# Kernel tuning notes

Measured on AMD Instinct MI355X. Metric: run time of the kernel, lower is better.

The kernel has to match this reference:

```python
import jax, jax.numpy as jnp
import numpy as np

B, T, C = 4, 2048, 1024
E, K, HID = 8, 2, 4096  # n_expert, top-k, mult*dim


def setup_inputs() -> dict:
    key = jax.random.key(0)
    ks = jax.random.split(key, 9)
    s = 1.0 / np.sqrt(C)
    sh = 1.0 / np.sqrt(HID)
    return {
        "x": jax.random.normal(ks[0], (B, T, C), jnp.float32),
        "wg_w": jax.random.normal(ks[1], (C, E), jnp.float32) * s,
        "wg_b": jnp.zeros((E,), jnp.float32),
        "w1": jax.random.normal(ks[2], (E, C, HID), jnp.float32) * s,
        "b1": jnp.zeros((E, HID), jnp.float32),
        "w3": jax.random.normal(ks[3], (E, C, HID), jnp.float32) * s,
        "b3": jnp.zeros((E, HID), jnp.float32),
        "w2": jax.random.normal(ks[4], (E, HID, C), jnp.float32) * sh,
        "b2": jnp.zeros((E, C), jnp.float32),
    }


def reference(x, wg_w, wg_b, w1, b1, w3, b3, w2, b2):
    Bx, Tx, Cx = x.shape
    xf = x.reshape(-1, Cx)                       # (S, C)
    S = xf.shape[0]
    # --- TopKGate ---
    logits = xf @ wg_w + wg_b                    # (S, E)
    probs = jax.nn.softmax(logits, axis=-1)
    vals, idx = jax.lax.top_k(probs, K)          # (S, K)
    importance = probs.mean(axis=0)              # (E,)
    load = jnp.zeros((E,), probs.dtype).at[idx[:, 0]].add(1.0) / S
    aux = E * (importance * load).sum()
    # per-token per-expert combine weight (top-k ids are unique per row)
    w_full = jnp.zeros((S, E), probs.dtype).at[jnp.arange(S)[:, None], idx].add(vals)
    # --- experts: SwiGLU FFN, loop over small fixed E ---
    y = jnp.zeros_like(xf)
    for e in range(E):
        h = jax.nn.silu(xf @ w1[e] + b1[e]) * (xf @ w3[e] + b3[e])  # (S, HID)
        y = y + w_full[:, e:e + 1] * (h @ w2[e] + b2[e])
    return y.reshape(Bx, Tx, Cx), aux
```

## Files before the change

### kernel.cpp

```cpp
#include <hip/hip_runtime.h>

#define S_TOK 8192
#define C_DIM 1024
#define E_NUM 8
#define HID_DIM 4096

typedef unsigned short u16;
typedef __bf16 bf16x8 __attribute__((ext_vector_type(8)));
typedef float f32x4 __attribute__((ext_vector_type(4)));

__device__ __forceinline__ u16 f2bf(float f){
  union { float f; unsigned u; } v; v.f = f;
  unsigned r = v.u + 0x7fffu + ((v.u >> 16) & 1u);
  return (u16)(r >> 16);
}
__device__ __forceinline__ float bf2f(u16 b){
  union { unsigned u; float f; } v; v.u = ((unsigned)b) << 16; return v.f;
}

__device__ __forceinline__ void async_copy16(const void* g, void* l){
  __builtin_amdgcn_global_load_lds((const __attribute__((address_space(1))) void*)g,
                                   (__attribute__((address_space(3))) void*)l, 16, 0, 0);
}

__global__ __launch_bounds__(256) void gate_kernel(
    const float* __restrict__ x, const float* __restrict__ wg_w, const float* __restrict__ wg_b,
    u16* __restrict__ xb,
    int* __restrict__ top_idx, float* __restrict__ top_val,
    float* __restrict__ imp_sum, int* __restrict__ cnt_top1, int* __restrict__ counts)
{
  __shared__ float s_imp[E_NUM];
  __shared__ int   s_c1[E_NUM], s_cnt[E_NUM];
  if (threadIdx.x < E_NUM){ s_imp[threadIdx.x]=0.f; s_c1[threadIdx.x]=0; s_cnt[threadIdx.x]=0; }
  __syncthreads();

  int wid = threadIdx.x >> 6, lane = threadIdx.x & 63;
  int t = blockIdx.x * 4 + wid;
  const float4* xr4 = (const float4*)(x + (size_t)t * C_DIM);
  u16* xbr = xb + (size_t)t * C_DIM;
  float acc[E_NUM];
  #pragma unroll
  for (int e=0;e<E_NUM;e++) acc[e]=0.f;
  #pragma unroll
  for (int c4 = 0; c4 < C_DIM/4/64; c4++){
    int c = (c4*64 + lane);
    float4 xv = xr4[c];
    ushort4 o = make_ushort4(f2bf(xv.x), f2bf(xv.y), f2bf(xv.z), f2bf(xv.w));
    *(ushort4*)&xbr[c*4] = o;
    const float* wr = wg_w + (size_t)c * 4 * E_NUM;
    #pragma unroll
    for (int e=0;e<E_NUM;e++)
      acc[e] += xv.x*wr[e] + xv.y*wr[E_NUM+e] + xv.z*wr[2*E_NUM+e] + xv.w*wr[3*E_NUM+e];
  }
  #pragma unroll
  for (int e=0;e<E_NUM;e++){
    float v = acc[e];
    #pragma unroll
    for (int off=32; off>0; off>>=1) v += __shfl_xor(v, off, 64);
    acc[e] = v + wg_b[e];
  }
  float mx = acc[0];
  #pragma unroll
  for (int e=1;e<E_NUM;e++) mx = fmaxf(mx, acc[e]);
  float sum = 0.f;
  #pragma unroll
  for (int e=0;e<E_NUM;e++){ acc[e] = __expf(acc[e]-mx); sum += acc[e]; }
  float inv = 1.f/sum;
  #pragma unroll
  for (int e=0;e<E_NUM;e++) acc[e] *= inv;
  int i1=0; float v1=acc[0];
  #pragma unroll
  for (int e=1;e<E_NUM;e++) if (acc[e] > v1){ v1=acc[e]; i1=e; }
  int i2=-1; float v2=-1.f;
  #pragma unroll
  for (int e=0;e<E_NUM;e++) if (e!=i1 && acc[e] > v2){ v2=acc[e]; i2=e; }

  if (lane==0){
    top_idx[t*2+0]=i1; top_idx[t*2+1]=i2;
    top_val[t*2+0]=v1; top_val[t*2+1]=v2;
    #pragma unroll
    for (int e=0;e<E_NUM;e++) atomicAdd(&s_imp[e], acc[e]);
    atomicAdd(&s_c1[i1],1);
    atomicAdd(&s_cnt[i1],1); atomicAdd(&s_cnt[i2],1);
  }
  __syncthreads();
  if (threadIdx.x < E_NUM){
    atomicAdd(&imp_sum[threadIdx.x], s_imp[threadIdx.x]);
    atomicAdd(&cnt_top1[threadIdx.x], s_c1[threadIdx.x]);
    atomicAdd(&counts[threadIdx.x], s_cnt[threadIdx.x]);
  }
}

__global__ void scan_kernel(const int* __restrict__ counts, int* __restrict__ offsets,
                            int* __restrict__ cursor, const float* __restrict__ imp_sum,
                            const int* __restrict__ cnt_top1, float* __restrict__ aux_out)
{
  if (threadIdx.x==0 && blockIdx.x==0){
    int off=0;
    #pragma unroll
    for (int e=0;e<E_NUM;e++){ offsets[e]=off; cursor[e]=off; off+=counts[e]; }
    float aux=0.f;
    #pragma unroll
    for (int e=0;e<E_NUM;e++)
      aux += (imp_sum[e]/(float)S_TOK) * ((float)cnt_top1[e]/(float)S_TOK);
    aux_out[0] = aux * (float)E_NUM;
  }
}

__global__ __launch_bounds__(256) void scatter_kernel(
    const int* __restrict__ top_idx, const float* __restrict__ top_val,
    int* __restrict__ cursor, int* __restrict__ token_list, float* __restrict__ token_w,
    int* __restrict__ pos_of_slot)
{
  int t = blockIdx.x*256 + threadIdx.x;
  #pragma unroll
  for (int k=0;k<2;k++){
    int e = top_idx[t*2+k];
    int pos = atomicAdd(&cursor[e], 1);
    token_list[pos] = t;
    token_w[pos]    = top_val[t*2+k];
    pos_of_slot[t*2+k] = pos;
  }
}

__global__ __launch_bounds__(256) void transpose_kernel(const float* __restrict__ in, u16* __restrict__ out,
                                                        int R, int Cc)
{
  __shared__ float tile[64][129];
  int e = blockIdx.z;
  const float* src = in  + (size_t)e*R*Cc;
  u16*         dst = out + (size_t)e*R*Cc;
  int c0 = blockIdx.x*128, r0 = blockIdx.y*64;
  int tx = threadIdx.x, ty = threadIdx.y;
  #pragma unroll
  for (int i = ty; i < 64; i += 16){
    const float* s = &src[(size_t)(r0+i)*Cc + c0 + tx*8];
    float4 v0 = *(const float4*)&s[0];
    float4 v1 = *(const float4*)&s[4];
    tile[i][tx*8+0] = v0.x; tile[i][tx*8+1] = v0.y;
    tile[i][tx*8+2] = v0.z; tile[i][tx*8+3] = v0.w;
    tile[i][tx*8+4] = v1.x; tile[i][tx*8+5] = v1.y;
    tile[i][tx*8+6] = v1.z; tile[i][tx*8+7] = v1.w;
  }
  __syncthreads();
  #pragma unroll
  for (int i = ty; i < 128; i += 16){
    ushort4 o = make_ushort4(f2bf(tile[tx*4+0][i]), f2bf(tile[tx*4+1][i]),
                             f2bf(tile[tx*4+2][i]), f2bf(tile[tx*4+3][i]));
    *(ushort4*)&dst[(size_t)(c0+i)*R + r0 + tx*4] = o;
  }
}


__global__ __launch_bounds__(512,1) void gemm1_kernel(
    const u16* __restrict__ xb, const u16* __restrict__ w1t, const u16* __restrict__ w3t,
    const float* __restrict__ b1, const float* __restrict__ b3,
    const int* __restrict__ token_list, const int* __restrict__ offsets, const int* __restrict__ counts,
    u16* __restrict__ h)
{
  int e  = blockIdx.z;
  int Ne = counts[e];
  int m0 = blockIdx.y * 128;
  if (m0 >= Ne) return;
  int seg = offsets[e];
  int n0  = blockIdx.x * 128;

  __shared__ u16 lA [128*64];
  __shared__ u16 lB1[128*64];
  __shared__ u16 lB3[128*64];

  int tid = threadIdx.x;
  int wid = tid >> 6, lane = tid & 63;
  int wr = wid >> 2, wc = wid & 3;

  const int srcsw = (((lane&7) ^ ((lane>>3)&7))) * 8;

  size_t gA[2], gB[2];
  #pragma unroll
  for (int i=0;i<2;i++){
    int r  = wid*16 + i*8 + (lane>>3);
    int rr = m0 + r; if (rr > Ne-1) rr = Ne-1;
    int tok = token_list[seg + rr];
    gA[i] = (size_t)tok * C_DIM + srcsw;
    int n  = n0 + wid*16 + i*8 + (lane>>3);
    gB[i] = ((size_t)e*HID_DIM + n) * C_DIM + srcsw;
  }

  f32x4 acc1[4][2], acc3[4][2];
  #pragma unroll
  for (int a=0;a<4;a++)
    #pragma unroll
    for (int b=0;b<2;b++){ acc1[a][b] = (f32x4){0.f,0.f,0.f,0.f}; acc3[a][b] = (f32x4){0.f,0.f,0.f,0.f}; }

  for (int k0=0; k0<C_DIM; k0+=64){
    #pragma unroll
    for (int i=0;i<2;i++){
      int lds_off = (wid*16 + i*8) * 64;
      async_copy16(xb  + gA[i] + k0, &lA [lds_off]);
      async_copy16(w1t + gB[i] + k0, &lB1[lds_off]);
      async_copy16(w3t + gB[i] + k0, &lB3[lds_off]);
    }
    __syncthreads();
    #pragma unroll
    for (int ks=0; ks<2; ks++){
      int kkS = ((ks*4 + (lane>>4)) ^ (lane&7)) * 8;
      bf16x8 af[4], b1f[2], b3f[2];
      #pragma unroll
      for (int mi=0;mi<4;mi++) af[mi]  = *(const bf16x8*)&lA [(wr*64+mi*16+(lane&15))*64 + kkS];
      #pragma unroll
      for (int nj=0;nj<2;nj++){ b1f[nj] = *(const bf16x8*)&lB1[(wc*32+nj*16+(lane&15))*64 + kkS];
                                b3f[nj] = *(const bf16x8*)&lB3[(wc*32+nj*16+(lane&15))*64 + kkS]; }
      #pragma unroll
      for (int mi=0;mi<4;mi++)
        #pragma unroll
        for (int nj=0;nj<2;nj++){
          acc1[mi][nj] = __builtin_amdgcn_mfma_f32_16x16x32_bf16(af[mi], b1f[nj], acc1[mi][nj], 0,0,0);
          acc3[mi][nj] = __builtin_amdgcn_mfma_f32_16x16x32_bf16(af[mi], b3f[nj], acc3[mi][nj], 0,0,0);
        }
    }
    __syncthreads();
  }

  const float* b1p = b1 + (size_t)e*HID_DIM + n0;
  const float* b3p = b3 + (size_t)e*HID_DIM + n0;
  #pragma unroll
  for (int nj=0;nj<2;nj++){
    int nl = wc*32 + nj*16 + (lane&15);
    float bb1 = b1p[nl], bb3 = b3p[nl];
    #pragma unroll
    for (int mi=0;mi<4;mi++){
      #pragma unroll
      for (int r=0;r<4;r++){
        int ml = wr*64 + mi*16 + (lane>>4)*4 + r;
        int m  = m0 + ml;
        if (m < Ne){
          float a = acc1[mi][nj][r] + bb1;
          float b = acc3[mi][nj][r] + bb3;
          float hv = (a / (1.f + __expf(-a))) * b;
          h[(size_t)(seg+m)*HID_DIM + n0 + nl] = f2bf(hv);
        }
      }
    }
  }
}

__global__ __launch_bounds__(512,1) void gemm2_kernel(
    const u16* __restrict__ h, const u16* __restrict__ w2t, const float* __restrict__ b2,
    const float* __restrict__ token_w,
    const int* __restrict__ offsets, const int* __restrict__ counts,
    u16* __restrict__ ybuf)
{
  int e  = blockIdx.z;
  int Ne = counts[e];
  int m0 = blockIdx.y * 128;
  if (m0 >= Ne) return;
  int seg = offsets[e];
  int n0  = blockIdx.x * 256;

  __shared__ u16 lA[128*64];
  __shared__ u16 lB[256*64];
  int tid=threadIdx.x, wid=tid>>6, lane=tid&63, wr=wid>>2, wc=wid&3;

  const int srcsw = (((lane&7) ^ ((lane>>3)&7))) * 8;

  size_t gA[2], gB[4];
  #pragma unroll
  for (int i=0;i<2;i++){
    int r  = wid*16 + i*8 + (lane>>3);
    int rr = m0 + r; if (rr > Ne-1) rr = Ne-1;
    gA[i] = (size_t)(seg + rr)*HID_DIM + srcsw;
  }
  #pragma unroll
  for (int i=0;i<4;i++){
    int n  = n0 + i*64 + wid*8 + (lane>>3);
    gB[i] = ((size_t)e*C_DIM + n) * HID_DIM + srcsw;
  }

  f32x4 acc[4][4];
  #pragma unroll
  for (int a=0;a<4;a++)
    #pragma unroll
    for (int b=0;b<4;b++) acc[a][b] = (f32x4){0.f,0.f,0.f,0.f};

  for (int k0=0; k0<HID_DIM; k0+=64){
    #pragma unroll
    for (int i=0;i<2;i++)
      async_copy16(h   + gA[i] + k0, &lA[(wid*16 + i*8)*64]);
    #pragma unroll
    for (int i=0;i<4;i++)
      async_copy16(w2t + gB[i] + k0, &lB[(i*64 + wid*8)*64]);
    __syncthreads();
    #pragma unroll
    for (int ks=0; ks<2; ks++){
      int kkS = ((ks*4 + (lane>>4)) ^ (lane&7)) * 8;
      bf16x8 af[4], bf[4];
      #pragma unroll
      for (int mi=0;mi<4;mi++) af[mi] = *(const bf16x8*)&lA[(wr*64+mi*16+(lane&15))*64 + kkS];
      #pragma unroll
      for (int nj=0;nj<4;nj++) bf[nj] = *(const bf16x8*)&lB[(wc*64+nj*16+(lane&15))*64 + kkS];
      #pragma unroll
      for (int mi=0;mi<4;mi++)
        #pragma unroll
        for (int nj=0;nj<4;nj++)
          acc[mi][nj] = __builtin_amdgcn_mfma_f32_16x16x32_bf16(af[mi], bf[nj], acc[mi][nj], 0,0,0);
    }
    __syncthreads();
  }

  const float* b2p = b2 + (size_t)e*C_DIM + n0;
  #pragma unroll
  for (int mi=0;mi<4;mi++){
    #pragma unroll
    for (int r=0;r<4;r++){
      int ml = wr*64 + mi*16 + (lane>>4)*4 + r;
      int m  = m0 + ml;
      if (m < Ne){
        float w = token_w[seg+m];
        #pragma unroll
        for (int nj=0;nj<4;nj++){
          int nl = wc*64 + nj*16 + (lane&15);
          ybuf[(size_t)(seg+m)*C_DIM + n0 + nl] = f2bf((acc[mi][nj][r] + b2p[nl]) * w);
        }
      }
    }
  }
}

__global__ __launch_bounds__(256) void combine_kernel(
    const u16* __restrict__ ybuf, const int* __restrict__ pos_of_slot, float* __restrict__ y)
{
  int t = blockIdx.x;
  int p0 = pos_of_slot[t*2+0], p1 = pos_of_slot[t*2+1];
  int c = threadIdx.x;
  ushort4 a = ((const ushort4*)(ybuf + (size_t)p0*C_DIM))[c];
  ushort4 b = ((const ushort4*)(ybuf + (size_t)p1*C_DIM))[c];
  float4 o = make_float4(bf2f(a.x)+bf2f(b.x), bf2f(a.y)+bf2f(b.y),
                         bf2f(a.z)+bf2f(b.z), bf2f(a.w)+bf2f(b.w));
  ((float4*)(y + (size_t)t*C_DIM))[c] = o;
}

extern "C" void kernel_launch(void* const* d_in, const int* in_sizes, int n_in,
                              void* d_out, int out_size, void* d_ws, size_t ws_size,
                              hipStream_t stream)
{
  const float* x    = (const float*)d_in[0];
  const float* wg_w = (const float*)d_in[1];
  const float* wg_b = (const float*)d_in[2];
  const float* w1   = (const float*)d_in[3];
  const float* b1   = (const float*)d_in[4];
  const float* w3   = (const float*)d_in[5];
  const float* b3   = (const float*)d_in[6];
  const float* w2   = (const float*)d_in[7];
  const float* b2   = (const float*)d_in[8];

  float* y   = (float*)d_out;
  float* aux = y + (size_t)S_TOK*C_DIM;

  char* ws = (char*)d_ws;
  size_t off = 0;
  auto alloc = [&](size_t bytes) -> void* {
    void* p = ws + off;
    off += (bytes + 255) & ~(size_t)255;
    return p;
  };
  u16*  xb        = (u16*)  alloc((size_t)S_TOK*C_DIM*2);
  u16*  w1t       = (u16*)  alloc((size_t)E_NUM*HID_DIM*C_DIM*2);
  u16*  w3t       = (u16*)  alloc((size_t)E_NUM*HID_DIM*C_DIM*2);
  u16*  w2t       = (u16*)  alloc((size_t)E_NUM*C_DIM*HID_DIM*2);
  u16*  h         = (u16*)  alloc((size_t)S_TOK*2*HID_DIM*2);
  int*  token_list= (int*)  alloc((size_t)S_TOK*2*4);
  float* token_w  = (float*)alloc((size_t)S_TOK*2*4);
  int*  top_idx   = (int*)  alloc((size_t)S_TOK*2*4);
  float* top_val  = (float*)alloc((size_t)S_TOK*2*4);
  int*  pos_of_slot=(int*)  alloc((size_t)S_TOK*2*4);
  char* stats     = (char*) alloc(4096);
  float* imp_sum  = (float*)(stats);
  int*   cnt1     = (int*)  (stats + 64);
  int*   counts   = (int*)  (stats + 128);
  int*   offsets  = (int*)  (stats + 192);
  int*   cursor   = (int*)  (stats + 256);
  u16* ybuf = (u16*)w1t;
  (void)in_sizes; (void)n_in; (void)out_size; (void)ws_size;

  hipMemsetAsync(stats, 0, 512, stream);

  dim3 tb(16,16);
  transpose_kernel<<<dim3(HID_DIM/128, C_DIM/64, E_NUM), tb, 0, stream>>>(w1, w1t, C_DIM, HID_DIM);
  transpose_kernel<<<dim3(HID_DIM/128, C_DIM/64, E_NUM), tb, 0, stream>>>(w3, w3t, C_DIM, HID_DIM);
  transpose_kernel<<<dim3(C_DIM/128, HID_DIM/64, E_NUM), tb, 0, stream>>>(w2, w2t, HID_DIM, C_DIM);

  gate_kernel<<<S_TOK/4, 256, 0, stream>>>(x, wg_w, wg_b, xb, top_idx, top_val, imp_sum, cnt1, counts);
  scan_kernel<<<1, 64, 0, stream>>>(counts, offsets, cursor, imp_sum, cnt1, aux);
  scatter_kernel<<<S_TOK/256, 256, 0, stream>>>(top_idx, top_val, cursor, token_list, token_w, pos_of_slot);

  gemm1_kernel<<<dim3(HID_DIM/128, S_TOK/128, E_NUM), 512, 0, stream>>>(
      xb, w1t, w3t, b1, b3, token_list, offsets, counts, h);
  gemm2_kernel<<<dim3(C_DIM/256, S_TOK/128, E_NUM), 512, 0, stream>>>(
      h, w2t, b2, token_w, offsets, counts, ybuf);
  combine_kernel<<<S_TOK, 256, 0, stream>>>(ybuf, pos_of_slot, y);
}
```

Measured before the change: 802.6 us.

## Compact expert GEMM grids via padded offsets and merge weight transposes

Replaces the per-expert 3D grid (which launched S_TOK/128 row tiles per expert, most exiting early) with a flat grid of 136 row tiles over padded per-expert offsets. Each block locates its expert by searching pad_off. The w1/w3 transposes are merged into one launch, and the transpose write path now stores 8 bf16 values per thread. This removes many empty blocks and one launch, at the cost of a small expert lookup per block.

```diff
diff --git a/kernel.cpp b/kernel.cpp
--- a/kernel.cpp
+++ b/kernel.cpp
@@ -8,6 +8,7 @@
 typedef unsigned short u16;
 typedef __bf16 bf16x8 __attribute__((ext_vector_type(8)));
 typedef float f32x4 __attribute__((ext_vector_type(4)));
+typedef unsigned short ushort8v __attribute__((ext_vector_type(8)));
 
 __device__ __forceinline__ u16 f2bf(float f){
   union { float f; unsigned u; } v; v.f = f;
@@ -92,13 +93,19 @@
 }
 
 __global__ void scan_kernel(const int* __restrict__ counts, int* __restrict__ offsets,
-                            int* __restrict__ cursor, const float* __restrict__ imp_sum,
+                            int* __restrict__ cursor, int* __restrict__ pad_off,
+                            const float* __restrict__ imp_sum,
                             const int* __restrict__ cnt_top1, float* __restrict__ aux_out)
 {
   if (threadIdx.x==0 && blockIdx.x==0){
-    int off=0;
-    #pragma unroll
-    for (int e=0;e<E_NUM;e++){ offsets[e]=off; cursor[e]=off; off+=counts[e]; }
+    int off=0, poff=0;
+    #pragma unroll
+    for (int e=0;e<E_NUM;e++){
+      offsets[e]=off; cursor[e]=off; pad_off[e]=poff;
+      off += counts[e];
+      poff += ((counts[e]+127)>>7)<<7;
+    }
+    pad_off[E_NUM]=poff;
     float aux=0.f;
     #pragma unroll
     for (int e=0;e<E_NUM;e++)
@@ -123,15 +130,17 @@
   }
 }
 
-__global__ __launch_bounds__(256) void transpose_kernel(const float* __restrict__ in, u16* __restrict__ out,
-                                                        int R, int Cc)
+__global__ __launch_bounds__(256) void transpose2_kernel(
+    const float* __restrict__ in0, const float* __restrict__ in1,
+    u16* __restrict__ out0, u16* __restrict__ out1, int R, int Cc)
 {
   __shared__ float tile[64][129];
-  int e = blockIdx.z;
-  const float* src = in  + (size_t)e*R*Cc;
-  u16*         dst = out + (size_t)e*R*Cc;
+  int z = blockIdx.z;
+  int e = z & (E_NUM-1);
+  const float* src = (z < E_NUM ? in0 : in1) + (size_t)e*R*Cc;
+  u16*         dst = (z < E_NUM ? out0 : out1) + (size_t)e*R*Cc;
   int c0 = blockIdx.x*128, r0 = blockIdx.y*64;
-  int tx = threadIdx.x, ty = threadIdx.y;
+  int tx = threadIdx.x & 15, ty = threadIdx.x >> 4;
   #pragma unroll
   for (int i = ty; i < 64; i += 16){
     const float* s = &src[(size_t)(r0+i)*Cc + c0 + tx*8];
@@ -143,25 +152,35 @@
     tile[i][tx*8+6] = v1.z; tile[i][tx*8+7] = v1.w;
   }
   __syncthreads();
-  #pragma unroll
-  for (int i = ty; i < 128; i += 16){
-    ushort4 o = make_ushort4(f2bf(tile[tx*4+0][i]), f2bf(tile[tx*4+1][i]),
-                             f2bf(tile[tx*4+2][i]), f2bf(tile[tx*4+3][i]));
-    *(ushort4*)&dst[(size_t)(c0+i)*R + r0 + tx*4] = o;
-  }
-}
+  int u  = threadIdx.x;
+  int cg = u & 7;
+  int rb = u >> 3;
+  #pragma unroll
+  for (int j = 0; j < 4; j++){
+    int cr = rb + 32*j;
+    ushort8v o;
+    #pragma unroll
+    for (int q=0;q<8;q++) o[q] = f2bf(tile[cg*8+q][cr]);
+    *(ushort8v*)&dst[(size_t)(c0+cr)*R + r0 + cg*8] = o;
+  }
+}
+
 
 
 __global__ __launch_bounds__(512,1) void gemm1_kernel(
     const u16* __restrict__ xb, const u16* __restrict__ w1t, const u16* __restrict__ w3t,
     const float* __restrict__ b1, const float* __restrict__ b3,
-    const int* __restrict__ token_list, const int* __restrict__ offsets, const int* __restrict__ counts,
+    const int* __restrict__ token_list, const int* __restrict__ offsets,
+    const int* __restrict__ counts, const int* __restrict__ pad_off,
     u16* __restrict__ h)
 {
-  int e  = blockIdx.z;
-  int Ne = counts[e];
-  int m0 = blockIdx.y * 128;
-  if (m0 >= Ne) return;
+  int row0 = blockIdx.y * 128;
+  if (row0 >= pad_off[E_NUM]) return;
+  int e = 0;
+  #pragma unroll
+  for (int k=1;k<E_NUM;k++) if (row0 >= pad_off[k]) e = k;
+  int m0  = row0 - pad_off[e];
+  int Ne  = counts[e];
   int seg = offsets[e];
   int n0  = blockIdx.x * 128;
 
@@ -247,13 +266,16 @@
 __global__ __launch_bounds__(512,1) void gemm2_kernel(
     const u16* __restrict__ h, const u16* __restrict__ w2t, const float* __restrict__ b2,
     const float* __restrict__ token_w,
-    const int* __restrict__ offsets, const int* __restrict__ counts,
+    const int* __restrict__ offsets, const int* __restrict__ counts, const int* __restrict__ pad_off,
     u16* __restrict__ ybuf)
 {
-  int e  = blockIdx.z;
-  int Ne = counts[e];
-  int m0 = blockIdx.y * 128;
-  if (m0 >= Ne) return;
+  int row0 = blockIdx.y * 128;
+  if (row0 >= pad_off[E_NUM]) return;
+  int e = 0;
+  #pragma unroll
+  for (int k=1;k<E_NUM;k++) if (row0 >= pad_off[k]) e = k;
+  int m0  = row0 - pad_off[e];
+  int Ne  = counts[e];
   int seg = offsets[e];
   int n0  = blockIdx.x * 256;
 
@@ -379,23 +401,24 @@
   int*   counts   = (int*)  (stats + 128);
   int*   offsets  = (int*)  (stats + 192);
   int*   cursor   = (int*)  (stats + 256);
+  int*   pad_off  = (int*)  (stats + 320);
   u16* ybuf = (u16*)w1t;
   (void)in_sizes; (void)n_in; (void)out_size; (void)ws_size;
 
   hipMemsetAsync(stats, 0, 512, stream);
 
-  dim3 tb(16,16);
-  transpose_kernel<<<dim3(HID_DIM/128, C_DIM/64, E_NUM), tb, 0, stream>>>(w1, w1t, C_DIM, HID_DIM);
-  transpose_kernel<<<dim3(HID_DIM/128, C_DIM/64, E_NUM), tb, 0, stream>>>(w3, w3t, C_DIM, HID_DIM);
-  transpose_kernel<<<dim3(C_DIM/128, HID_DIM/64, E_NUM), tb, 0, stream>>>(w2, w2t, HID_DIM, C_DIM);
+  transpose2_kernel<<<dim3(HID_DIM/128, C_DIM/64, 2*E_NUM), 256, 0, stream>>>(
+      w1, w3, w1t, w3t, C_DIM, HID_DIM);
+  transpose2_kernel<<<dim3(C_DIM/128, HID_DIM/64, E_NUM), 256, 0, stream>>>(
+      w2, w2, w2t, w2t, HID_DIM, C_DIM);
 
   gate_kernel<<<S_TOK/4, 256, 0, stream>>>(x, wg_w, wg_b, xb, top_idx, top_val, imp_sum, cnt1, counts);
-  scan_kernel<<<1, 64, 0, stream>>>(counts, offsets, cursor, imp_sum, cnt1, aux);
+  scan_kernel<<<1, 64, 0, stream>>>(counts, offsets, cursor, pad_off, imp_sum, cnt1, aux);
   scatter_kernel<<<S_TOK/256, 256, 0, stream>>>(top_idx, top_val, cursor, token_list, token_w, pos_of_slot);
 
-  gemm1_kernel<<<dim3(HID_DIM/128, S_TOK/128, E_NUM), 512, 0, stream>>>(
-      xb, w1t, w3t, b1, b3, token_list, offsets, counts, h);
-  gemm2_kernel<<<dim3(C_DIM/256, S_TOK/128, E_NUM), 512, 0, stream>>>(
-      h, w2t, b2, token_w, offsets, counts, ybuf);
+  gemm1_kernel<<<dim3(HID_DIM/128, 136), 512, 0, stream>>>(
+      xb, w1t, w3t, b1, b3, token_list, offsets, counts, pad_off, h);
+  gemm2_kernel<<<dim3(C_DIM/256, 136), 512, 0, stream>>>(
+      h, w2t, b2, token_w, offsets, counts, pad_off, ybuf);
   combine_kernel<<<S_TOK, 256, 0, stream>>>(ybuf, pos_of_slot, y);
 }
```

Measured after the change: 795.9 us. Within noise of the previous version (-0.8%).
